# Optimization experiments

Measured on AMD Instinct MI355X. Metric: run time of the kernel, lower is better.

The kernel has to match this reference:

```python
import jax, jax.numpy as jnp
import numpy as np

NUM_BLOCKS = 8
D = 1024          # residual_dim == attention_dim
FF = 4096         # feed_forward_dim
B, S = 4, 4096
EPS_ATTN = 1e-6
EPS_LN = 1e-6


def _ln(x, scale, bias):
    m = jnp.mean(x, axis=-1, keepdims=True)
    v = jnp.var(x, axis=-1, keepdims=True)
    return (x - m) * jax.lax.rsqrt(v + EPS_LN) * scale + bias


def setup_inputs() -> dict:
    key = jax.random.key(0)
    ks = jax.random.split(key, 16)
    g = lambda k, shape, fan: jax.random.normal(k, shape, jnp.float32) * (1.0 / np.sqrt(fan))
    inp = {
        "x": jax.random.normal(ks[0], (B, S, D), jnp.float32),
        "Wq": g(ks[1], (NUM_BLOCKS, D, D), D), "bq": jnp.zeros((NUM_BLOCKS, D), jnp.float32),
        "Wk": g(ks[2], (NUM_BLOCKS, D, D), D), "bk": jnp.zeros((NUM_BLOCKS, D), jnp.float32),
        "Wv": g(ks[3], (NUM_BLOCKS, D, D), D), "bv": jnp.zeros((NUM_BLOCKS, D), jnp.float32),
        "Wo": g(ks[4], (NUM_BLOCKS, D, D), D), "bo": jnp.zeros((NUM_BLOCKS, D), jnp.float32),
        "ln1_s": jnp.ones((NUM_BLOCKS, D), jnp.float32), "ln1_b": jnp.zeros((NUM_BLOCKS, D), jnp.float32),
        "W1": g(ks[5], (NUM_BLOCKS, D, FF), D), "b1": jnp.zeros((NUM_BLOCKS, FF), jnp.float32),
        "W2": g(ks[6], (NUM_BLOCKS, FF, D), FF), "b2": jnp.zeros((NUM_BLOCKS, D), jnp.float32),
        "ln2_s": jnp.ones((NUM_BLOCKS, D), jnp.float32), "ln2_b": jnp.zeros((NUM_BLOCKS, D), jnp.float32),
    }
    return inp


def _forward(x, Wq, bq, Wk, bk, Wv, bv, Wo, bo, ln1_s, ln1_b, W1, b1, W2, b2, ln2_s, ln2_b):
    gelu = lambda t: jax.nn.gelu(t, approximate=True)  # flax nn.gelu default
    fmap = lambda t: jax.nn.elu(t) + 1.0
    for i in range(NUM_BLOCKS):
        # --- linear attention sublayer ---
        residual = x
        Q = fmap(x @ Wq[i] + bq[i])          # [b, s, h]
        K = fmap(x @ Wk[i] + bk[i])          # [b, s, h]
        value = x @ Wv[i] + bv[i]            # [b, s, h]
        KV = jnp.einsum('nsh,nsh->nh', K, value)          # per-channel sum_s K*V
        Ksum = jnp.sum(K, axis=1)                         # [b, h]
        Z = 1.0 / (Q * Ksum[:, None, :] + EPS_ATTN)       # [b, s, h]
        V = Q * KV[:, None, :] * Z                        # [b, s, h]
        attn_out = gelu(V @ Wo[i] + bo[i])
        x = _ln(attn_out + residual, ln1_s[i], ln1_b[i])
        # --- feed-forward sublayer ---
        residual = x
        h = gelu(x @ W1[i] + b1[i])
        ff_out = gelu(h @ W2[i] + b2[i])
        x = _ln(ff_out + residual, ln2_s[i], ln2_b[i])
    return x


def reference(x, Wq, bq, Wk, bk, Wv, bv, Wo, bo, ln1_s, ln1_b, W1, b1, W2, b2, ln2_s, ln2_b):
    return _forward(x, Wq, bq, Wk, bk, Wv, bv, Wo, bo, ln1_s, ln1_b, W1, b1, W2, b2, ln2_s, ln2_b)
```

## Files before the change

### kernel.cpp

```cpp
#include <hip/hip_runtime.h>
#include <hip/hip_bf16.h>
#include <cstdint>

typedef unsigned short ushort_t;
typedef __attribute__((ext_vector_type(8))) short short8;
typedef __attribute__((ext_vector_type(4))) float floatx4;
typedef __attribute__((ext_vector_type(4))) ushort_t ushort4v;

#define DEVI __device__ __forceinline__

DEVI float b2f(ushort_t u){ union{unsigned int i; float f;} v; v.i = ((unsigned int)u)<<16; return v.f; }
DEVI ushort_t f2b(float f){ union{float f; unsigned int i;} v; v.f=f; unsigned int r = (v.i + 0x7FFFu + ((v.i>>16)&1u)) >> 16; return (ushort_t)r; }

DEVI float gelu_f(float t){
  float t3 = t*t*t;
  return 0.5f*t*(1.0f + tanhf(0.7978845608028654f*(t + 0.044715f*t3)));
}

#define GLD_LDS16(src, dst) \
  __builtin_amdgcn_global_load_lds((const __attribute__((address_space(1))) void*)(src), \
                                   (__attribute__((address_space(3))) void*)(dst), 16, 0, 0)

#define BAR()    asm volatile("s_barrier" ::: "memory")
#define WAITV(n) asm volatile("s_waitcnt vmcnt(" #n ")" ::: "memory")

DEVI void gemm_core(const ushort_t* __restrict__ A, const ushort_t* __restrict__ Bt,
                    int K, int tileM, int tileN, floatx4 (&acc)[8][4])
{
  __shared__ alignas(16) ushort_t As[2][16384];
  __shared__ alignas(16) ushort_t Bs[2][16384];
  const int tid  = threadIdx.x;
  const int wave = tid >> 6, lane = tid & 63;
  const int quad = lane >> 4, l16 = lane & 15;
  const int wm = wave >> 2, wn = wave & 3;

  const int rr = tid >> 3;
  const int gg = (tid & 7) ^ (rr & 7);
  const ushort_t* srcA = A  + (size_t)(tileM + rr) * K + gg * 8;
  const ushort_t* srcB = Bt + (size_t)(tileN + rr) * K + gg * 8;
  const size_t K64 = (size_t)K * 64;
  ushort_t* dstA = &As[0][0] + wave * 512;
  ushort_t* dstB = &Bs[0][0] + wave * 512;

#define STAGE_R(t, r) do{ \
    const ushort_t* s_ = (((r) < 2) ? srcA : srcB) + (size_t)(t) * 64 + (((r) & 1) ? 2*K64 : (size_t)0); \
    ushort_t* d_ = (((r) < 2) ? dstA : dstB) + (((t) & 1) ? 16384 : 0) + (((r) & 1) ? 8192 : 0); \
    GLD_LDS16(s_,       d_); \
    GLD_LDS16(s_ + K64, d_ + 4096); \
  }while(0)

#define PHASE_MFMA(n0, n1) \
    BAR(); \
    __builtin_amdgcn_s_setprio(1); \
    _Pragma("unroll") \
    for (int mi = 0; mi < 8; mi++){ \
      acc[mi][n0] = __builtin_amdgcn_mfma_f32_16x16x32_bf16(af[mi], bf0, acc[mi][n0], 0, 0, 0); \
      acc[mi][n1] = __builtin_amdgcn_mfma_f32_16x16x32_bf16(af[mi], bf1, acc[mi][n1], 0, 0, 0); \
    } \
    __builtin_amdgcn_s_setprio(0); \
    BAR()

  const int nkt = K >> 6;
  STAGE_R(0, 0); STAGE_R(0, 1); STAGE_R(0, 2); STAGE_R(0, 3);
  if (nkt > 1){
    STAGE_R(1, 0); STAGE_R(1, 1); STAGE_R(1, 2);
    WAITV(6);
  } else {
    WAITV(0);
  }
  BAR();

  const int s0   = (quad ^ (l16 & 7)) * 8;
  const int aRow = (wm * 128 + l16) * 64;
  const int bRow = (wn * 64  + l16) * 64;

  for (int t = 0; t < nkt; ++t){
    const ushort_t* as = &As[t & 1][0];
    const ushort_t* bs = &Bs[t & 1][0];
    if (t + 1 < nkt) STAGE_R(t + 1, 3);

    short8 af[8], bf0, bf1;
    #pragma unroll
    for (int mi = 0; mi < 8; mi++) af[mi] = *(const short8*)(as + aRow + mi * 1024 + s0);
    bf0 = *(const short8*)(bs + bRow + s0);
    bf1 = *(const short8*)(bs + bRow + 1024 + s0);
    PHASE_MFMA(0, 1);
    bf0 = *(const short8*)(bs + bRow + 2 * 1024 + s0);
    bf1 = *(const short8*)(bs + bRow + 3 * 1024 + s0);
    PHASE_MFMA(2, 3);
    {
      const int s1 = s0 ^ 32;
      #pragma unroll
      for (int mi = 0; mi < 8; mi++) af[mi] = *(const short8*)(as + aRow + mi * 1024 + s1);
      bf0 = *(const short8*)(bs + bRow + s1);
      bf1 = *(const short8*)(bs + bRow + 1024 + s1);
      PHASE_MFMA(0, 1);
      bf0 = *(const short8*)(bs + bRow + 2 * 1024 + s1);
      bf1 = *(const short8*)(bs + bRow + 3 * 1024 + s1);
      PHASE_MFMA(2, 3);
    }
    if (t + 2 < nkt){
      STAGE_R(t + 2, 0); STAGE_R(t + 2, 1); STAGE_R(t + 2, 2);
      WAITV(6);
      BAR();
    } else if (t + 1 < nkt){
      WAITV(0);
      BAR();
    }
  }
#undef STAGE_R
#undef PHASE_MFMA
}

template<int EPI>
__global__ __launch_bounds__(512, 2)
void gemm_kernel(const ushort_t* __restrict__ A, const ushort_t* __restrict__ Bt,
                 const float* __restrict__ bias, const float* __restrict__ res,
                 ushort_t* __restrict__ out, int N, int K)
{
  const int tileM = blockIdx.x * 256, tileN = blockIdx.y * 256;
  floatx4 acc[8][4] = {};
  gemm_core(A, Bt, K, tileM, tileN, acc);

  const int tid = threadIdx.x, wave = tid >> 6, lane = tid & 63;
  const int quad = lane >> 4, l16 = lane & 15;
  const int wm = wave >> 2, wn = wave & 3;

  float bv4[4];
  #pragma unroll
  for (int ni = 0; ni < 4; ni++) bv4[ni] = bias[tileN + wn * 64 + ni * 16 + l16];

  #pragma unroll
  for (int mi = 0; mi < 8; mi++){
    #pragma unroll
    for (int r = 0; r < 4; r++){
      const int row = tileM + wm * 128 + mi * 16 + quad * 4 + r;
      #pragma unroll
      for (int ni = 0; ni < 4; ni++){
        const int col = tileN + wn * 64 + ni * 16 + l16;
        float v = acc[mi][ni][r] + bv4[ni];
        if constexpr (EPI == 0){ v = (v > 0.f) ? (v + 1.f) : expf(v); }
        else if constexpr (EPI == 2){ v = gelu_f(v); }
        else if constexpr (EPI == 3){ v = gelu_f(v) + res[(size_t)row * N + col]; }
        out[(size_t)row * N + col] = f2b(v);
      }
    }
  }
}

__global__ __launch_bounds__(512, 2)
void qkv_gemm_kernel(const ushort_t* __restrict__ A, const ushort_t* __restrict__ Bt,
                     const float* __restrict__ bq, const float* __restrict__ bk,
                     const float* __restrict__ bv,
                     ushort_t* __restrict__ outQ, ushort_t* __restrict__ outK,
                     ushort_t* __restrict__ outV, int K)
{
  const int tileM = blockIdx.x * 256, tileN = blockIdx.y * 256;
  floatx4 acc[8][4] = {};
  gemm_core(A, Bt, K, tileM, tileN, acc);

  const int tid = threadIdx.x, wave = tid >> 6, lane = tid & 63;
  const int quad = lane >> 4, l16 = lane & 15;
  const int wm = wave >> 2, wn = wave & 3;

  const int seg  = tileN >> 10;
  const int nloc = tileN & 1023;
  const float* bias = (seg == 0) ? bq : (seg == 1) ? bk : bv;
  ushort_t* out     = (seg == 0) ? outQ : (seg == 1) ? outK : outV;

  float bv4[4];
  #pragma unroll
  for (int ni = 0; ni < 4; ni++) bv4[ni] = bias[nloc + wn * 64 + ni * 16 + l16];

  #pragma unroll
  for (int mi = 0; mi < 8; mi++){
    #pragma unroll
    for (int r = 0; r < 4; r++){
      const int row = tileM + wm * 128 + mi * 16 + quad * 4 + r;
      #pragma unroll
      for (int ni = 0; ni < 4; ni++){
        const int col = nloc + wn * 64 + ni * 16 + l16;
        float v = acc[mi][ni][r] + bv4[ni];
        if (seg < 2){ v = (v > 0.f) ? (v + 1.f) : expf(v); }
        out[(size_t)row * 1024 + col] = f2b(v);
      }
    }
  }
}

__global__ __launch_bounds__(256)
void reduce_kv_kernel(const ushort_t* __restrict__ Kb, const ushort_t* __restrict__ Vb,
                      float* __restrict__ KV, float* __restrict__ Ksum)
{
  const int b = blockIdx.x >> 6, chunk = blockIdx.x & 63;
  const int t = threadIdx.x;
  const size_t base = ((size_t)b*4096 + (size_t)chunk*64)*1024 + t*4;
  float kv[4] = {0,0,0,0}, ks[4] = {0,0,0,0};
  for (int s = 0; s < 64; s++){
    ushort4v kk = *(const ushort4v*)(Kb + base + (size_t)s*1024);
    ushort4v vv = *(const ushort4v*)(Vb + base + (size_t)s*1024);
    #pragma unroll
    for (int j = 0; j < 4; j++){ float kf = b2f(kk[j]); kv[j] += kf*b2f(vv[j]); ks[j] += kf; }
  }
  #pragma unroll
  for (int j = 0; j < 4; j++){
    atomicAdd(&KV[b*1024 + t*4 + j], kv[j]);
    atomicAdd(&Ksum[b*1024 + t*4 + j], ks[j]);
  }
}

__global__ __launch_bounds__(256)
void attn_map_kernel(ushort_t* __restrict__ Q, const float* __restrict__ KV, const float* __restrict__ Ksum)
{
  const size_t g = (size_t)blockIdx.x*256 + threadIdx.x;
  const size_t base = g*4;
  const int b  = (int)(base >> 22);
  const int h0 = (int)(base & 1023);
  ushort4v q4 = *(const ushort4v*)(Q + base);
  ushort4v o4;
  #pragma unroll
  for (int j = 0; j < 4; j++){
    float q = b2f(q4[j]);
    float v = q*KV[b*1024 + h0 + j] / (q*Ksum[b*1024 + h0 + j] + 1e-6f);
    o4[j] = f2b(v);
  }
  *(ushort4v*)(Q + base) = o4;
}

__global__ __launch_bounds__(256)
void ln_kernel(const ushort_t* __restrict__ y, const float* __restrict__ sc,
               const float* __restrict__ bi, ushort_t* __restrict__ xb, float* __restrict__ xf)
{
  const int row = blockIdx.x, t = threadIdx.x;
  const ushort_t* yr = y + (size_t)row*1024;
  ushort4v v4 = *(const ushort4v*)(yr + t*4);
  float f[4]; float s1 = 0.f, s2 = 0.f;
  #pragma unroll
  for (int j = 0; j < 4; j++){ f[j] = b2f(v4[j]); s1 += f[j]; s2 += f[j]*f[j]; }
  #pragma unroll
  for (int off = 32; off; off >>= 1){ s1 += __shfl_down(s1, off); s2 += __shfl_down(s2, off); }
  __shared__ float red[2][4];
  const int wave = t >> 6, lane = t & 63;
  if (lane == 0){ red[0][wave] = s1; red[1][wave] = s2; }
  __syncthreads();
  s1 = red[0][0] + red[0][1] + red[0][2] + red[0][3];
  s2 = red[1][0] + red[1][1] + red[1][2] + red[1][3];
  const float mean = s1 * (1.0f/1024.0f);
  const float var  = s2 * (1.0f/1024.0f) - mean*mean;
  const float inv  = rsqrtf(var + 1e-6f);
  ushort4v o4;
  #pragma unroll
  for (int j = 0; j < 4; j++){
    const int h = t*4 + j;
    const float o = (f[j] - mean)*inv*sc[h] + bi[h];
    o4[j] = f2b(o);
    xf[(size_t)row*1024 + h] = o;
  }
  *(ushort4v*)(xb + (size_t)row*1024 + t*4) = o4;
}

struct TParams { const float* src[6]; ushort_t* dst[6]; };

__global__ __launch_bounds__(256)
void transpose_all_kernel(TParams p)
{
  __shared__ float tile[32][33];
  const int id = blockIdx.x;
  int m, bx, by, R, C;
  if (id < 4096){ m = 4; int l = id;        bx = l & 127; by = l >> 7; R = 1024; C = 4096; }
  else if (id < 8192){ m = 5; int l = id - 4096; bx = l & 31; by = l >> 5; R = 4096; C = 1024; }
  else { int l = id - 8192; m = l >> 10; l &= 1023; bx = l & 31; by = l >> 5; R = 1024; C = 1024; }
  const float* in = p.src[m];
  ushort_t* out = p.dst[m];
  const int t = threadIdx.x;
  const int tx = t & 31, ty = t >> 5;
  const int rb = by*32, cb = bx*32;
  #pragma unroll
  for (int j = 0; j < 32; j += 8) tile[ty+j][tx] = in[(size_t)(rb+ty+j)*C + cb+tx];
  __syncthreads();
  #pragma unroll
  for (int j = 0; j < 32; j += 8) out[(size_t)(cb+ty+j)*R + rb+tx] = f2b(tile[tx][ty+j]);
}

__global__ __launch_bounds__(256)
void cvt_kernel(const float* __restrict__ in, ushort_t* __restrict__ out)
{
  const size_t base = ((size_t)blockIdx.x*256 + threadIdx.x)*4;
  ushort4v o4;
  #pragma unroll
  for (int j = 0; j < 4; j++) o4[j] = f2b(in[base + j]);
  *(ushort4v*)(out + base) = o4;
}

extern "C" void kernel_launch(void* const* d_in, const int* in_sizes, int n_in,
                              void* d_out, int out_size, void* d_ws, size_t ws_size,
                              hipStream_t stream)
{
  const float* x_in = (const float*)d_in[0];
  const float* Wq   = (const float*)d_in[1];
  const float* bq   = (const float*)d_in[2];
  const float* Wk   = (const float*)d_in[3];
  const float* bk   = (const float*)d_in[4];
  const float* Wv   = (const float*)d_in[5];
  const float* bv   = (const float*)d_in[6];
  const float* Wo   = (const float*)d_in[7];
  const float* bo   = (const float*)d_in[8];
  const float* ln1s = (const float*)d_in[9];
  const float* ln1b = (const float*)d_in[10];
  const float* W1   = (const float*)d_in[11];
  const float* b1   = (const float*)d_in[12];
  const float* W2   = (const float*)d_in[13];
  const float* b2   = (const float*)d_in[14];
  const float* ln2s = (const float*)d_in[15];
  const float* ln2b = (const float*)d_in[16];

  float* xf = (float*)d_out;

  char* ws = (char*)d_ws;
  const size_t MB = 1024*1024;
  ushort_t* xb     = (ushort_t*)(ws);
  char*     regB   = ws + 32*MB;
  ushort_t* bufQ   = (ushort_t*)(regB);
  ushort_t* bufK   = (ushort_t*)(regB + 32*MB);
  ushort_t* bufVal = (ushort_t*)(regB + 64*MB);
  ushort_t* bufH   = (ushort_t*)(regB);
  ushort_t* bufY   = (ushort_t*)(regB + 128*MB);
  ushort_t* WqkvT  = (ushort_t*)(ws + 192*MB);
  ushort_t* WoT    = (ushort_t*)(ws + 198*MB);
  ushort_t* W1T    = (ushort_t*)(ws + 200*MB);
  ushort_t* W2T    = (ushort_t*)(ws + 208*MB);
  float*    KV     = (float*)(ws + 216*MB);
  float*    Ksum   = (float*)(ws + 216*MB + 16*1024);

  const int M = 16384, D = 1024, FF = 4096;
  const dim3 blk(256);
  const dim3 blkG(512);

  hipMemcpyAsync(xf, x_in, (size_t)M*D*sizeof(float), hipMemcpyDeviceToDevice, stream);
  cvt_kernel<<<dim3(M*D/1024), blk, 0, stream>>>(x_in, xb);

  for (int i = 0; i < 8; i++){
    TParams tp;
    tp.src[0] = Wq + (size_t)i*D*D;  tp.dst[0] = WqkvT;
    tp.src[1] = Wk + (size_t)i*D*D;  tp.dst[1] = WqkvT + 1024*1024;
    tp.src[2] = Wv + (size_t)i*D*D;  tp.dst[2] = WqkvT + 2*1024*1024;
    tp.src[3] = Wo + (size_t)i*D*D;  tp.dst[3] = WoT;
    tp.src[4] = W1 + (size_t)i*D*FF; tp.dst[4] = W1T;
    tp.src[5] = W2 + (size_t)i*FF*D; tp.dst[5] = W2T;
    transpose_all_kernel<<<dim3(12288), blk, 0, stream>>>(tp);

    qkv_gemm_kernel<<<dim3(64, 12), blkG, 0, stream>>>(xb, WqkvT, bq + i*D, bk + i*D, bv + i*D,
                                                       bufQ, bufK, bufVal, D);

    hipMemsetAsync(KV, 0, 32*1024, stream);
    reduce_kv_kernel<<<dim3(256), blk, 0, stream>>>(bufK, bufVal, KV, Ksum);
    attn_map_kernel<<<dim3(16384), blk, 0, stream>>>(bufQ, KV, Ksum);

    gemm_kernel<3><<<dim3(64, 4), blkG, 0, stream>>>(bufQ, WoT, bo + i*D, xf, bufVal, D, D);
    ln_kernel<<<dim3(16384), blk, 0, stream>>>(bufVal, ln1s + i*D, ln1b + i*D, xb, xf);

    gemm_kernel<2><<<dim3(64, 16), blkG, 0, stream>>>(xb, W1T, b1 + i*FF, nullptr, bufH, FF, D);
    gemm_kernel<3><<<dim3(64, 4),  blkG, 0, stream>>>(bufH, W2T, b2 + i*D, xf, bufY, D, FF);
    ln_kernel<<<dim3(16384), blk, 0, stream>>>(bufY, ln2s + i*D, ln2b + i*D, xb, xf);
  }
  (void)in_sizes; (void)n_in; (void)out_size; (void)ws_size;
}
```

Measured before the change: 6.403 ms.

## Unroll GEMM K-loop by two with compile-time buffer offsets and prefetched fragments

Restructures the GEMM main loop to process two K-tiles per iteration, using a templated ktile helper with compile-time LDS buffer offsets instead of runtime t&1 indexing. Inside each tile, all four B fragments are loaded up front, and the second-half A/B fragments are loaded while the first-half MFMAs are still pending. This hides LDS read latency behind MFMA work and removes address arithmetic. It raises register pressure from the extra fragment arrays, which could hurt occupancy under the 512x2 launch bounds. The loop also assumes nkt is even or handles the tail only partially.

New measurement: 6.594 ms. 1.03x slower.

```diff
diff --git a/kernel.cpp b/kernel.cpp
--- a/kernel.cpp
+++ b/kernel.cpp
@@ -23,6 +23,48 @@
 
 #define BAR()    asm volatile("s_barrier" ::: "memory")
 #define WAITV(n) asm volatile("s_waitcnt vmcnt(" #n ")" ::: "memory")
+
+#define MFMA16(d, a, b) d = __builtin_amdgcn_mfma_f32_16x16x32_bf16(a, b, d, 0, 0, 0)
+
+template<int BUFOFF>
+DEVI void ktile(const ushort_t* aB0, const ushort_t* aB1,
+                const ushort_t* bB0, const ushort_t* bB1, floatx4 (&acc)[8][4])
+{
+  short8 af0[8], af1[8], bf0[4], bf1[4];
+  #pragma unroll
+  for (int mi = 0; mi < 8; mi++) af0[mi] = *(const short8*)(aB0 + BUFOFF + mi*1024);
+  #pragma unroll
+  for (int ni = 0; ni < 4; ni++) bf0[ni] = *(const short8*)(bB0 + BUFOFF + ni*1024);
+  BAR();
+  __builtin_amdgcn_s_setprio(1);
+  #pragma unroll
+  for (int mi = 0; mi < 8; mi++){ MFMA16(acc[mi][0], af0[mi], bf0[0]); MFMA16(acc[mi][1], af0[mi], bf0[1]); }
+  __builtin_amdgcn_s_setprio(0);
+  BAR();
+  #pragma unroll
+  for (int mi = 0; mi < 8; mi++) af1[mi] = *(const short8*)(aB1 + BUFOFF + mi*1024);
+  bf1[0] = *(const short8*)(bB1 + BUFOFF);
+  bf1[1] = *(const short8*)(bB1 + BUFOFF + 1024);
+  BAR();
+  __builtin_amdgcn_s_setprio(1);
+  #pragma unroll
+  for (int mi = 0; mi < 8; mi++){ MFMA16(acc[mi][2], af0[mi], bf0[2]); MFMA16(acc[mi][3], af0[mi], bf0[3]); }
+  __builtin_amdgcn_s_setprio(0);
+  BAR();
+  bf1[2] = *(const short8*)(bB1 + BUFOFF + 2048);
+  bf1[3] = *(const short8*)(bB1 + BUFOFF + 3072);
+  BAR();
+  __builtin_amdgcn_s_setprio(1);
+  #pragma unroll
+  for (int mi = 0; mi < 8; mi++){ MFMA16(acc[mi][0], af1[mi], bf1[0]); MFMA16(acc[mi][1], af1[mi], bf1[1]); }
+  __builtin_amdgcn_s_setprio(0);
+  BAR();
+  __builtin_amdgcn_s_setprio(1);
+  #pragma unroll
+  for (int mi = 0; mi < 8; mi++){ MFMA16(acc[mi][2], af1[mi], bf1[2]); MFMA16(acc[mi][3], af1[mi], bf1[3]); }
+  __builtin_amdgcn_s_setprio(0);
+  BAR();
+}
 
 DEVI void gemm_core(const ushort_t* __restrict__ A, const ushort_t* __restrict__ Bt,
                     int K, int tileM, int tileN, floatx4 (&acc)[8][4])
@@ -42,74 +84,54 @@
   ushort_t* dstA = &As[0][0] + wave * 512;
   ushort_t* dstB = &Bs[0][0] + wave * 512;
 
-#define STAGE_R(t, r) do{ \
-    const ushort_t* s_ = (((r) < 2) ? srcA : srcB) + (size_t)(t) * 64 + (((r) & 1) ? 2*K64 : (size_t)0); \
-    ushort_t* d_ = (((r) < 2) ? dstA : dstB) + (((t) & 1) ? 16384 : 0) + (((r) & 1) ? 8192 : 0); \
-    GLD_LDS16(s_,       d_); \
-    GLD_LDS16(s_ + K64, d_ + 4096); \
-  }while(0)
-
-#define PHASE_MFMA(n0, n1) \
-    BAR(); \
-    __builtin_amdgcn_s_setprio(1); \
-    _Pragma("unroll") \
-    for (int mi = 0; mi < 8; mi++){ \
-      acc[mi][n0] = __builtin_amdgcn_mfma_f32_16x16x32_bf16(af[mi], bf0, acc[mi][n0], 0, 0, 0); \
-      acc[mi][n1] = __builtin_amdgcn_mfma_f32_16x16x32_bf16(af[mi], bf1, acc[mi][n1], 0, 0, 0); \
-    } \
-    __builtin_amdgcn_s_setprio(0); \
-    BAR()
+#define STAGE2(sp, dp) do{ GLD_LDS16((sp), (dp)); GLD_LDS16((sp) + K64, (dp) + 4096); }while(0)
+
+  const int s0 = (quad ^ (l16 & 7)) * 8;
+  const int s1 = s0 ^ 32;
+  const ushort_t* aB0 = &As[0][0] + (wm*128 + l16)*64 + s0;
+  const ushort_t* aB1 = &As[0][0] + (wm*128 + l16)*64 + s1;
+  const ushort_t* bB0 = &Bs[0][0] + (wn*64  + l16)*64 + s0;
+  const ushort_t* bB1 = &Bs[0][0] + (wn*64  + l16)*64 + s1;
 
   const int nkt = K >> 6;
-  STAGE_R(0, 0); STAGE_R(0, 1); STAGE_R(0, 2); STAGE_R(0, 3);
+
+  STAGE2(srcA,              dstA);
+  STAGE2(srcA + 2*K64,      dstA + 8192);
+  STAGE2(srcB,              dstB);
+  STAGE2(srcB + 2*K64,      dstB + 8192);
   if (nkt > 1){
-    STAGE_R(1, 0); STAGE_R(1, 1); STAGE_R(1, 2);
+    STAGE2(srcA + 64,          dstA + 16384);
+    STAGE2(srcA + 64 + 2*K64,  dstA + 16384 + 8192);
+    STAGE2(srcB + 64,          dstB + 16384);
     WAITV(6);
   } else {
     WAITV(0);
   }
   BAR();
 
-  const int s0   = (quad ^ (l16 & 7)) * 8;
-  const int aRow = (wm * 128 + l16) * 64;
-  const int bRow = (wn * 64  + l16) * 64;
-
-  for (int t = 0; t < nkt; ++t){
-    const ushort_t* as = &As[t & 1][0];
-    const ushort_t* bs = &Bs[t & 1][0];
-    if (t + 1 < nkt) STAGE_R(t + 1, 3);
-
-    short8 af[8], bf0, bf1;
-    #pragma unroll
-    for (int mi = 0; mi < 8; mi++) af[mi] = *(const short8*)(as + aRow + mi * 1024 + s0);
-    bf0 = *(const short8*)(bs + bRow + s0);
-    bf1 = *(const short8*)(bs + bRow + 1024 + s0);
-    PHASE_MFMA(0, 1);
-    bf0 = *(const short8*)(bs + bRow + 2 * 1024 + s0);
-    bf1 = *(const short8*)(bs + bRow + 3 * 1024 + s0);
-    PHASE_MFMA(2, 3);
-    {
-      const int s1 = s0 ^ 32;
-      #pragma unroll
-      for (int mi = 0; mi < 8; mi++) af[mi] = *(const short8*)(as + aRow + mi * 1024 + s1);
-      bf0 = *(const short8*)(bs + bRow + s1);
-      bf1 = *(const short8*)(bs + bRow + 1024 + s1);
-      PHASE_MFMA(0, 1);
-      bf0 = *(const short8*)(bs + bRow + 2 * 1024 + s1);
-      bf1 = *(const short8*)(bs + bRow + 3 * 1024 + s1);
-      PHASE_MFMA(2, 3);
+  for (int tt = 0; tt < nkt; tt += 2){
+    STAGE2(srcB + (size_t)(tt+1)*64 + 2*K64, dstB + 16384 + 8192);
+    ktile<0>(aB0, aB1, bB0, bB1, acc);
+    if (tt + 2 < nkt){
+      const size_t k8 = (size_t)(tt+2) * 64;
+      STAGE2(srcA + k8,          dstA);
+      STAGE2(srcA + k8 + 2*K64,  dstA + 8192);
+      STAGE2(srcB + k8,          dstB);
+      WAITV(6); BAR();
+      STAGE2(srcB + k8 + 2*K64,  dstB + 8192);
+    } else {
+      WAITV(0); BAR();
     }
-    if (t + 2 < nkt){
-      STAGE_R(t + 2, 0); STAGE_R(t + 2, 1); STAGE_R(t + 2, 2);
-      WAITV(6);
-      BAR();
-    } else if (t + 1 < nkt){
-      WAITV(0);
-      BAR();
+    ktile<16384>(aB0, aB1, bB0, bB1, acc);
+    if (tt + 3 < nkt){
+      const size_t k8 = (size_t)(tt+3) * 64;
+      STAGE2(srcA + k8,          dstA + 16384);
+      STAGE2(srcA + k8 + 2*K64,  dstA + 16384 + 8192);
+      STAGE2(srcB + k8,          dstB + 16384);
+      WAITV(6); BAR();
     }
   }
-#undef STAGE_R
-#undef PHASE_MFMA
+#undef STAGE2
 }
 
 template<int EPI>
```
